# Optimization experiments

Measured on AMD Instinct MI355X. Metric: run time of the kernel, lower is better.

The kernel has to match this reference:

```python
import jax, jax.numpy as jnp
import numpy as np

EPS = 1e-06


def setup_inputs() -> dict:
    key = jax.random.key(0)
    kq, kk, kv = jax.random.split(key, 3)
    shape = (4, 16, 4096, 64)  # [batch, heads, seq, head_dim]
    q = jax.random.normal(kq, shape, dtype=jnp.float32)
    k = jax.random.normal(kk, shape, dtype=jnp.float32)
    v = jax.random.normal(kv, shape, dtype=jnp.float32)
    return {"q": q, "k": k, "v": v}


def reference(q, k, v):
    # elu(x)+1 feature map (positive kernel)
    q_prime = jax.nn.elu(q) + 1.0  # [b,h,s,d]
    k_prime = jax.nn.elu(k) + 1.0  # [b,h,s,d]
    # KV aggregate: [b,h,d,d] -- avoids the [s,s] score matrix
    kv_agg = jnp.einsum('bhsd,bhse->bhde', k_prime, v)
    num = jnp.einsum('bhsd,bhde->bhse', q_prime, kv_agg)  # [b,h,s,d]
    k_sum = k_prime.sum(axis=-2)                           # [b,h,d]
    denom = jnp.einsum('bhsd,bhd->bhs', q_prime, k_sum)[..., None] + EPS
    return num / denom
```

## Files before the change

kernel.cpp:

```cpp
#include <hip/hip_runtime.h>


#define EPS_LA 1e-6f

constexpr int BH = 64;
constexpr int SEQ = 4096;
constexpr int DIM = 64;
constexpr int KVELEM = DIM * DIM + DIM;
constexpr int NPB = 32;
constexpr int SUBT = 2;
constexpr int SCH = SEQ / NPB;

typedef short bf16x8 __attribute__((ext_vector_type(8)));
typedef float f32x4 __attribute__((ext_vector_type(4)));

__device__ __forceinline__ float elu1(float x) {
    return x > 0.f ? x + 1.f : __expf(x);
}
__device__ __forceinline__ void elu4(float4& v) {
    v.x = elu1(v.x); v.y = elu1(v.y); v.z = elu1(v.z); v.w = elu1(v.w);
}

__device__ __forceinline__ unsigned int f2bf(float x) {
    unsigned int u = __float_as_uint(x);
    return (u + 0x7fffu + ((u >> 16) & 1u)) >> 16;
}
__device__ __forceinline__ unsigned int pack2bf(float lo, float hi) {
    return f2bf(lo) | (f2bf(hi) << 16);
}

__device__ __forceinline__ int swz(int d, int s2) {
    return d * 32 + (s2 ^ ((((d >> 1) ^ (d >> 2)) & 7) << 2));
}

template<bool ATOMIC>
__global__ __launch_bounds__(256, 6) void kv_mfma_kernel(
    const float* __restrict__ K, const float* __restrict__ V,
    float* __restrict__ dst) {
    const int bh = blockIdx.y;
    const int blk = blockIdx.x;
    const int t = threadIdx.x;
    const int w = t >> 6, l = t & 63;

    __shared__ unsigned int KT[64 * 32];
    __shared__ unsigned int VT[64 * 32];
    __shared__ float csumS[4][64];

    const float* Kb = K + ((size_t)bh * SEQ + (size_t)blk * SCH) * DIM;
    const float* Vb = V + ((size_t)bh * SEQ + (size_t)blk * SCH) * DIM;

    const int c0 = (t & 15) * 4;
    const int lg = l >> 4;
    const int lr = l & 15;

    f32x4 acc[4];
    #pragma unroll
    for (int m = 0; m < 4; ++m)
        #pragma unroll
        for (int r = 0; r < 4; ++r) acc[m][r] = 0.f;

    float cs0 = 0.f, cs1 = 0.f, cs2 = 0.f, cs3 = 0.f;

    #pragma unroll
    for (int st = 0; st < SUBT; ++st) {
        const float* Ks = Kb + (size_t)st * 64 * DIM;
        const float* Vs = Vb + (size_t)st * 64 * DIM;

        #pragma unroll
        for (int i = 0; i < 2; ++i) {
            const int p = (t >> 4) + 16 * i;
            float4 ka = *(const float4*)(Ks + (size_t)(2 * p) * DIM + c0);
            float4 kb = *(const float4*)(Ks + (size_t)(2 * p + 1) * DIM + c0);
            const float4 va = *(const float4*)(Vs + (size_t)(2 * p) * DIM + c0);
            const float4 vb = *(const float4*)(Vs + (size_t)(2 * p + 1) * DIM + c0);
            elu4(ka); elu4(kb);
            cs0 += ka.x + kb.x; cs1 += ka.y + kb.y;
            cs2 += ka.z + kb.z; cs3 += ka.w + kb.w;
            KT[swz(c0 + 0, p)] = pack2bf(ka.x, kb.x);
            KT[swz(c0 + 1, p)] = pack2bf(ka.y, kb.y);
            KT[swz(c0 + 2, p)] = pack2bf(ka.z, kb.z);
            KT[swz(c0 + 3, p)] = pack2bf(ka.w, kb.w);
            VT[swz(c0 + 0, p)] = pack2bf(va.x, vb.x);
            VT[swz(c0 + 1, p)] = pack2bf(va.y, vb.y);
            VT[swz(c0 + 2, p)] = pack2bf(va.z, vb.z);
            VT[swz(c0 + 3, p)] = pack2bf(va.w, vb.w);
        }

        if (st == SUBT - 1) {
            cs0 += __shfl_xor(cs0, 16); cs0 += __shfl_xor(cs0, 32);
            cs1 += __shfl_xor(cs1, 16); cs1 += __shfl_xor(cs1, 32);
            cs2 += __shfl_xor(cs2, 16); cs2 += __shfl_xor(cs2, 32);
            cs3 += __shfl_xor(cs3, 16); cs3 += __shfl_xor(cs3, 32);
            if (l < 16) *(float4*)&csumS[w][l * 4] = make_float4(cs0, cs1, cs2, cs3);
        }
        __syncthreads();

        #pragma unroll
        for (int ks = 0; ks < 2; ++ks) {
            const int s2b = ks * 16 + lg * 4;
            const bf16x8 bfrag =
                *reinterpret_cast<const bf16x8*>(&VT[swz(16 * w + lr, s2b)]);
            #pragma unroll
            for (int m = 0; m < 4; ++m) {
                const bf16x8 afrag =
                    *reinterpret_cast<const bf16x8*>(&KT[swz(16 * m + lr, s2b)]);
                acc[m] = __builtin_amdgcn_mfma_f32_16x16x32_bf16(afrag, bfrag, acc[m],
                                                                 0, 0, 0);
            }
        }
        if (st < SUBT - 1) __syncthreads();
    }

    float* wout = ATOMIC ? dst + (size_t)bh * KVELEM
                         : dst + ((size_t)blk * BH + bh) * KVELEM;

    if (t < 64) {
        const float s = csumS[0][t] + csumS[1][t] + csumS[2][t] + csumS[3][t];
        if (ATOMIC) atomicAdd(&wout[DIM * DIM + t], s);
        else        wout[DIM * DIM + t] = s;
    }

    #pragma unroll
    for (int m = 0; m < 4; ++m) {
        #pragma unroll
        for (int r = 0; r < 4; ++r) {
            const int d = 16 * m + 4 * lg + r;
            const int e = 16 * w + lr;
            if (ATOMIC) atomicAdd(&wout[(size_t)d * DIM + e], acc[m][r]);
            else        wout[(size_t)d * DIM + e] = acc[m][r];
        }
    }
}

__global__ __launch_bounds__(256) void reduce_partials_kernel(
    const float* __restrict__ partial, float* __restrict__ fin) {
    const int bh = blockIdx.y;
    const int j = blockIdx.x * 256 + threadIdx.x;
    if (j >= KVELEM) return;
    float s = 0.f;
    #pragma unroll
    for (int c = 0; c < NPB; ++c)
        s += partial[((size_t)c * BH + bh) * KVELEM + j];
    fin[(size_t)bh * KVELEM + j] = s;
}

__global__ __launch_bounds__(256) void out_kernel(
    const float* __restrict__ Q, const float* __restrict__ ws,
    float* __restrict__ out) {
    const int bh = blockIdx.y;
    const int rb = blockIdx.x;
    const int wave = threadIdx.x >> 6, lane = threadIdx.x & 63;
    const int t = threadIdx.x;
    const int tr = lane >> 3;
    const int tc = lane & 7;

    const float* w = ws + (size_t)bh * KVELEM;
    const float* Qw = Q + ((size_t)bh * SEQ + (size_t)rb * 128 + (size_t)wave * 32) * DIM;
    float* Ow = out + ((size_t)bh * SEQ + (size_t)rb * 128 + (size_t)wave * 32) * DIM;

    __shared__ float kvS[DIM][DIM];
    __shared__ float ksumS[DIM];
    __shared__ float qS[4][32][DIM];

    #pragma unroll
    for (int i = 0; i < 4; ++i) {
        const int idx = (i * 256 + t) * 4;
        *(float4*)&kvS[idx >> 6][idx & 63] = *(const float4*)(w + idx);
    }
    if (t < DIM) ksumS[t] = w[DIM * DIM + t];

    #pragma unroll
    for (int it = 0; it < 8; ++it) {
        const int row = it * 4 + (lane >> 4);
        const int cc = lane & 15;
        float4 qv = *(const float4*)(Qw + (size_t)row * DIM + cc * 4);
        elu4(qv);
        *(float4*)&qS[wave][row][((cc ^ ((row >> 2) & 7)) & 15) * 4] = qv;
    }
    __syncthreads();

    float acc[4][8] = {{0.f}};
    float accd[4] = {0.f, 0.f, 0.f, 0.f};

    #pragma unroll 2
    for (int dc = 0; dc < 16; ++dc) {
        float4 qv[4];
        #pragma unroll
        for (int i = 0; i < 4; ++i)
            qv[i] = *(const float4*)&qS[wave][tr * 4 + i][((dc ^ tr) & 15) * 4];
        const float4 ks = *(const float4*)&ksumS[dc * 4];
        #pragma unroll
        for (int dd = 0; dd < 4; ++dd) {
            const int d = dc * 4 + dd;
            const float4 ka = *(const float4*)&kvS[d][tc * 8];
            const float4 kb = *(const float4*)&kvS[d][tc * 8 + 4];
            const float ksd = (&ks.x)[dd];
            #pragma unroll
            for (int i = 0; i < 4; ++i) {
                const float qq = (&qv[i].x)[dd];
                accd[i] += qq * ksd;
                acc[i][0] += qq * ka.x; acc[i][1] += qq * ka.y;
                acc[i][2] += qq * ka.z; acc[i][3] += qq * ka.w;
                acc[i][4] += qq * kb.x; acc[i][5] += qq * kb.y;
                acc[i][6] += qq * kb.z; acc[i][7] += qq * kb.w;
            }
        }
    }

    #pragma unroll
    for (int i = 0; i < 4; ++i) {
        const float inv = 1.f / (accd[i] + EPS_LA);
        float4 o0, o1;
        o0.x = acc[i][0] * inv; o0.y = acc[i][1] * inv;
        o0.z = acc[i][2] * inv; o0.w = acc[i][3] * inv;
        o1.x = acc[i][4] * inv; o1.y = acc[i][5] * inv;
        o1.z = acc[i][6] * inv; o1.w = acc[i][7] * inv;
        float* orow = Ow + (size_t)(tr * 4 + i) * DIM + tc * 8;
        *(float4*)(orow) = o0;
        *(float4*)(orow + 4) = o1;
    }
}

extern "C" void kernel_launch(void* const* d_in, const int* in_sizes, int n_in,
                              void* d_out, int out_size, void* d_ws, size_t ws_size,
                              hipStream_t stream) {
    const float* q = (const float*)d_in[0];
    const float* k = (const float*)d_in[1];
    const float* v = (const float*)d_in[2];
    float* out = (float*)d_out;
    float* ws = (float*)d_ws;

    const size_t partial_elems = (size_t)NPB * BH * KVELEM;
    const size_t need = (partial_elems + (size_t)BH * KVELEM) * sizeof(float);

    dim3 blk(256);
    const float* fin_ptr;
    if (ws_size >= need) {
        float* partial = ws;
        float* fin = ws + partial_elems;
        hipLaunchKernelGGL((kv_mfma_kernel<false>), dim3(NPB, BH), blk, 0, stream,
                           k, v, partial);
        hipLaunchKernelGGL(reduce_partials_kernel, dim3((KVELEM + 255) / 256, BH),
                           blk, 0, stream, partial, fin);
        fin_ptr = fin;
    } else {
        float* fin = ws;
        hipMemsetAsync(fin, 0, (size_t)BH * KVELEM * sizeof(float), stream);
        hipLaunchKernelGGL((kv_mfma_kernel<true>), dim3(NPB, BH), blk, 0, stream,
                           k, v, fin);
        fin_ptr = fin;
    }
    hipLaunchKernelGGL(out_kernel, dim3(SEQ / 128, BH), blk, 0, stream,
                       q, fin_ptr, out);
}
```

Before: 82.05 us.

## Double-buffer K/V tile loads in registers and LDS, halve blocks per head

Halves the number of sequence chunks per head, so each block processes four 64-row tiles instead of two. It prefetches the next tile's K/V into registers while the current tile is transformed and fed to MFMA. Ping-pong LDS buffers replace the second barrier per iteration. This aims to hide global-load latency and cut the partial-KV reduction traffic, at the cost of more registers and LDS, lower occupancy (launch bound 6 to 4), and fewer blocks in flight.

```diff
diff --git a/kernel.cpp b/kernel.cpp
--- a/kernel.cpp
+++ b/kernel.cpp
@@ -7,9 +7,9 @@
 constexpr int SEQ = 4096;
 constexpr int DIM = 64;
 constexpr int KVELEM = DIM * DIM + DIM;
-constexpr int NPB = 32;
-constexpr int SUBT = 2;
+constexpr int NPB = 16;
 constexpr int SCH = SEQ / NPB;
+constexpr int NT = SCH / 64;
 
 typedef short bf16x8 __attribute__((ext_vector_type(8)));
 typedef float f32x4 __attribute__((ext_vector_type(4)));
@@ -34,7 +34,7 @@
 }
 
 template<bool ATOMIC>
-__global__ __launch_bounds__(256, 6) void kv_mfma_kernel(
+__global__ __launch_bounds__(256, 4) void kv_mfma_kernel(
     const float* __restrict__ K, const float* __restrict__ V,
     float* __restrict__ dst) {
     const int bh = blockIdx.y;
@@ -42,14 +42,15 @@
     const int t = threadIdx.x;
     const int w = t >> 6, l = t & 63;
 
-    __shared__ unsigned int KT[64 * 32];
-    __shared__ unsigned int VT[64 * 32];
+    __shared__ unsigned int KT[2][64 * 32];
+    __shared__ unsigned int VT[2][64 * 32];
     __shared__ float csumS[4][64];
 
     const float* Kb = K + ((size_t)bh * SEQ + (size_t)blk * SCH) * DIM;
     const float* Vb = V + ((size_t)bh * SEQ + (size_t)blk * SCH) * DIM;
 
     const int c0 = (t & 15) * 4;
+    const int pr = t >> 4;
     const int lg = l >> 4;
     const int lr = l & 15;
 
@@ -61,54 +62,78 @@
 
     float cs0 = 0.f, cs1 = 0.f, cs2 = 0.f, cs3 = 0.f;
 
-    #pragma unroll
-    for (int st = 0; st < SUBT; ++st) {
-        const float* Ks = Kb + (size_t)st * 64 * DIM;
-        const float* Vs = Vb + (size_t)st * 64 * DIM;
+    float4 ka[2][2], kb[2][2], va[2][2], vb[2][2];
+
+    #pragma unroll
+    for (int i = 0; i < 2; ++i) {
+        const int p = pr + 16 * i;
+        const float* Ks = Kb + (size_t)(2 * p) * DIM + c0;
+        const float* Vs = Vb + (size_t)(2 * p) * DIM + c0;
+        ka[0][i] = *(const float4*)Ks;
+        kb[0][i] = *(const float4*)(Ks + DIM);
+        va[0][i] = *(const float4*)Vs;
+        vb[0][i] = *(const float4*)(Vs + DIM);
+    }
+
+    #pragma unroll
+    for (int st = 0; st < NT; ++st) {
+        const int cur = st & 1;
+        const int nxt = cur ^ 1;
+
+        if (st + 1 < NT) {
+            #pragma unroll
+            for (int i = 0; i < 2; ++i) {
+                const int p = pr + 16 * i;
+                const float* Ks = Kb + ((size_t)(st + 1) * 64 + 2 * p) * DIM + c0;
+                const float* Vs = Vb + ((size_t)(st + 1) * 64 + 2 * p) * DIM + c0;
+                ka[nxt][i] = *(const float4*)Ks;
+                kb[nxt][i] = *(const float4*)(Ks + DIM);
+                va[nxt][i] = *(const float4*)Vs;
+                vb[nxt][i] = *(const float4*)(Vs + DIM);
+            }
+        }
 
         #pragma unroll
         for (int i = 0; i < 2; ++i) {
-            const int p = (t >> 4) + 16 * i;
-            float4 ka = *(const float4*)(Ks + (size_t)(2 * p) * DIM + c0);
-            float4 kb = *(const float4*)(Ks + (size_t)(2 * p + 1) * DIM + c0);
-            const float4 va = *(const float4*)(Vs + (size_t)(2 * p) * DIM + c0);
-            const float4 vb = *(const float4*)(Vs + (size_t)(2 * p + 1) * DIM + c0);
-            elu4(ka); elu4(kb);
-            cs0 += ka.x + kb.x; cs1 += ka.y + kb.y;
-            cs2 += ka.z + kb.z; cs3 += ka.w + kb.w;
-            KT[swz(c0 + 0, p)] = pack2bf(ka.x, kb.x);
-            KT[swz(c0 + 1, p)] = pack2bf(ka.y, kb.y);
-            KT[swz(c0 + 2, p)] = pack2bf(ka.z, kb.z);
-            KT[swz(c0 + 3, p)] = pack2bf(ka.w, kb.w);
-            VT[swz(c0 + 0, p)] = pack2bf(va.x, vb.x);
-            VT[swz(c0 + 1, p)] = pack2bf(va.y, vb.y);
-            VT[swz(c0 + 2, p)] = pack2bf(va.z, vb.z);
-            VT[swz(c0 + 3, p)] = pack2bf(va.w, vb.w);
-        }
-
-        if (st == SUBT - 1) {
+            const int p = pr + 16 * i;
+            float4 kka = ka[cur][i], kkb = kb[cur][i];
+            elu4(kka); elu4(kkb);
+            cs0 += kka.x + kkb.x; cs1 += kka.y + kkb.y;
+            cs2 += kka.z + kkb.z; cs3 += kka.w + kkb.w;
+            KT[cur][swz(c0 + 0, p)] = pack2bf(kka.x, kkb.x);
+            KT[cur][swz(c0 + 1, p)] = pack2bf(kka.y, kkb.y);
+            KT[cur][swz(c0 + 2, p)] = pack2bf(kka.z, kkb.z);
+            KT[cur][swz(c0 + 3, p)] = pack2bf(kka.w, kkb.w);
+            const float4 vva = va[cur][i], vvb = vb[cur][i];
+            VT[cur][swz(c0 + 0, p)] = pack2bf(vva.x, vvb.x);
+            VT[cur][swz(c0 + 1, p)] = pack2bf(vva.y, vvb.y);
+            VT[cur][swz(c0 + 2, p)] = pack2bf(vva.z, vvb.z);
+            VT[cur][swz(c0 + 3, p)] = pack2bf(vva.w, vvb.w);
+        }
+
+        if (st == NT - 1) {
             cs0 += __shfl_xor(cs0, 16); cs0 += __shfl_xor(cs0, 32);
             cs1 += __shfl_xor(cs1, 16); cs1 += __shfl_xor(cs1, 32);
             cs2 += __shfl_xor(cs2, 16); cs2 += __shfl_xor(cs2, 32);
             cs3 += __shfl_xor(cs3, 16); cs3 += __shfl_xor(cs3, 32);
             if (l < 16) *(float4*)&csumS[w][l * 4] = make_float4(cs0, cs1, cs2, cs3);
         }
+
         __syncthreads();
 
         #pragma unroll
-        for (int ks = 0; ks < 2; ++ks) {
-            const int s2b = ks * 16 + lg * 4;
+        for (int ks2 = 0; ks2 < 2; ++ks2) {
+            const int s2b = ks2 * 16 + lg * 4;
             const bf16x8 bfrag =
-                *reinterpret_cast<const bf16x8*>(&VT[swz(16 * w + lr, s2b)]);
+                *reinterpret_cast<const bf16x8*>(&VT[cur][swz(16 * w + lr, s2b)]);
             #pragma unroll
             for (int m = 0; m < 4; ++m) {
                 const bf16x8 afrag =
-                    *reinterpret_cast<const bf16x8*>(&KT[swz(16 * m + lr, s2b)]);
+                    *reinterpret_cast<const bf16x8*>(&KT[cur][swz(16 * m + lr, s2b)]);
                 acc[m] = __builtin_amdgcn_mfma_f32_16x16x32_bf16(afrag, bfrag, acc[m],
                                                                  0, 0, 0);
             }
         }
-        if (st < SUBT - 1) __syncthreads();
     }
 
     float* wout = ATOMIC ? dst + (size_t)bh * KVELEM
```

Result: faster. 73.68 us (-10.2%).
